# Kernel tuning notes

Hardware: AMD Instinct MI355X
Metric: run time of the kernel (lower is better)

## Reference

```python
import jax, jax.numpy as jnp
import numpy as np

B = 16        # molecules per batch (equal-size segments)
N = 2048      # atoms per molecule
EPS = 1e-09   # module epsilon added to distances
TINY = 1e-16  # jitter inside sqrt to keep grads finite on the masked diagonal


def setup_inputs() -> dict:
    key = jax.random.key(0)
    k1, k2 = jax.random.split(key)
    positions = jax.random.normal(k1, (B * N, 3), dtype=jnp.float32) * 5.0  # [BN,3]
    q = jax.random.normal(k2, (B * N, 1), dtype=jnp.float32)                # [BN,1]
    batch = jnp.repeat(jnp.arange(B, dtype=jnp.int32), N)                   # [BN], sorted equal segments
    return {"positions": positions, "q": q, "batch": batch}


def reference(positions, q, batch):
    # Equal-size segments: the per-molecule python loop in the torch module
    # becomes a batched [B,N,...] computation (batch ids are sorted, N per mol).
    r = positions.reshape(B, N, 3)
    qb = q.reshape(B, N, 1)

    diff = r[:, :, None, :] - r[:, None, :, :]                    # [B,N,N,3]
    dist = jnp.sqrt(jnp.sum(diff * diff, axis=-1) + TINY) + EPS   # [B,N,N]
    dist = dist[..., None]                                        # [B,N,N,1]

    mask = (1.0 - jnp.eye(N, dtype=positions.dtype))[..., None]   # [N,N,1] zero diagonal

    # q_i * q_j / |r_i - r_j|, self-interaction masked, double-count halved
    pot = mask * (qb[:, :, None, :] * qb[:, None, :, :] / dist)   # [B,N,N,1]
    pot_per_mol = pot.sum(axis=(1, 2)) * 0.5                      # [B, n_q=1]
    coulomb_potential = pot_per_mol.sum(axis=1)                   # [B] (aggregation 'sum')

    # field_j = sum_i q_i / |r_i - r_j|  (norm_factor = 1.0)
    field = (qb[:, :, None, :] / dist * mask).sum(axis=1)         # [B,N,1]
    q_field = field.reshape(B * N, 1)                             # [BN,1]

    return coulomb_potential, q_field
```

## Files before the change

### kernel.cpp

```cpp
#include <hip/hip_runtime.h>

#define NB 16
#define NA 2048
#define BLOCK 256
#define JL 8
#define JT 4
#define JB (JL*JT)
#define SPLIT 32
#define RSTRIDE 33

__global__ void zero_pot_kernel(float* out) {
    if (threadIdx.x < NB) out[threadIdx.x] = 0.0f;
}

__global__ __launch_bounds__(BLOCK) void coulomb_kernel(
    const float* __restrict__ pos,
    const float* __restrict__ q,
    float* __restrict__ out)
{
    __shared__ float4 sp4[NA];
    __shared__ float red[SPLIT * RSTRIDE];

    const int t = threadIdx.x;
    const int blocksPerMol = NA / JB;
    const int mol   = blockIdx.x / blocksPerMol;
    const int jBase = (blockIdx.x % blocksPerMol) * JB;
    const long molAtom = (long)mol * NA;

    for (int k = t; k < NA; k += BLOCK) {
        const long a = molAtom + k;
        sp4[k] = make_float4(pos[a*3+0], pos[a*3+1], pos[a*3+2], q[a]);
    }
    __syncthreads();

    const int jl  = t & (JL - 1);
    const int sid = t >> 3;
    const int j0  = jBase + jl;

    float4 jp[JT];
    int    jidx[JT];
    #pragma unroll
    for (int m = 0; m < JT; ++m) {
        jidx[m] = j0 + m * JL;
        jp[m]   = sp4[jidx[m]];
    }

    float acc[JT] = {0.0f, 0.0f, 0.0f, 0.0f};

    #pragma unroll 4
    for (int k = 0; k < NA / SPLIT; ++k) {
        const int i = k * SPLIT + sid;
        const float4 p = sp4[i];
        #pragma unroll
        for (int m = 0; m < JT; ++m) {
            float dx = p.x - jp[m].x;
            float dy = p.y - jp[m].y;
            float dz = p.z - jp[m].z;
            float d2 = fmaf(dx, dx, fmaf(dy, dy, fmaf(dz, dz, 1e-16f)));
            float inv = __builtin_amdgcn_rsqf(d2);
            float qs  = (i == jidx[m]) ? 0.0f : p.w;
            acc[m] = fmaf(qs, inv, acc[m]);
        }
    }

    #pragma unroll
    for (int m = 0; m < JT; ++m)
        red[sid * RSTRIDE + jl + m * JL] = acc[m];
    __syncthreads();

    if (t < JB) {
        float field = 0.0f;
        #pragma unroll
        for (int s = 0; s < SPLIT; ++s) field += red[s * RSTRIDE + t];

        out[NB + molAtom + jBase + t] = field;

        float pot = 0.5f * sp4[jBase + t].w * field;
        #pragma unroll
        for (int off = 16; off > 0; off >>= 1)
            pot += __shfl_down(pot, off, 32);
        if (t == 0) atomicAdd(&out[mol], pot);
    }
}

extern "C" void kernel_launch(void* const* d_in, const int* in_sizes, int n_in,
                              void* d_out, int out_size, void* d_ws, size_t ws_size,
                              hipStream_t stream) {
    const float* pos = (const float*)d_in[0];
    const float* q   = (const float*)d_in[1];
    float* out = (float*)d_out;

    zero_pot_kernel<<<1, 64, 0, stream>>>(out);

    const int grid = NB * (NA / JB);
    coulomb_kernel<<<grid, BLOCK, 0, stream>>>(pos, q, out);
}
```

Baseline: 80.05 us.

## Prepack float4 atoms in workspace and read from global instead of LDS staging

```diff
diff --git a/kernel.cpp b/kernel.cpp
--- a/kernel.cpp
+++ b/kernel.cpp
@@ -7,42 +7,39 @@
 #define JT 4
 #define JB (JL*JT)
 #define SPLIT 32
-#define RSTRIDE 33
 
-__global__ void zero_pot_kernel(float* out) {
-    if (threadIdx.x < NB) out[threadIdx.x] = 0.0f;
+__global__ void pack_zero_kernel(const float* __restrict__ pos,
+                                 const float* __restrict__ q,
+                                 float4* __restrict__ pk,
+                                 float* __restrict__ out) {
+    const int a = blockIdx.x * blockDim.x + threadIdx.x;
+    pk[a] = make_float4(pos[a*3+0], pos[a*3+1], pos[a*3+2], q[a]);
+    if (blockIdx.x == 0 && threadIdx.x < NB) out[threadIdx.x] = 0.0f;
 }
 
 __global__ __launch_bounds__(BLOCK) void coulomb_kernel(
-    const float* __restrict__ pos,
-    const float* __restrict__ q,
+    const float4* __restrict__ pk,
     float* __restrict__ out)
 {
-    __shared__ float4 sp4[NA];
-    __shared__ float red[SPLIT * RSTRIDE];
+    __shared__ float red[4 * JB];
 
     const int t = threadIdx.x;
     const int blocksPerMol = NA / JB;
     const int mol   = blockIdx.x / blocksPerMol;
     const int jBase = (blockIdx.x % blocksPerMol) * JB;
     const long molAtom = (long)mol * NA;
+    const float4* mp = pk + molAtom;
 
-    for (int k = t; k < NA; k += BLOCK) {
-        const long a = molAtom + k;
-        sp4[k] = make_float4(pos[a*3+0], pos[a*3+1], pos[a*3+2], q[a]);
-    }
-    __syncthreads();
-
-    const int jl  = t & (JL - 1);
-    const int sid = t >> 3;
-    const int j0  = jBase + jl;
+    const int jl   = t & (JL - 1);
+    const int sid  = t >> 3;
+    const int wave = t >> 6;
 
     float4 jp[JT];
     int    jidx[JT];
     #pragma unroll
     for (int m = 0; m < JT; ++m) {
-        jidx[m] = j0 + m * JL;
-        jp[m]   = sp4[jidx[m]];
+        jidx[m] = jBase + jl + m * JL;
+        jp[m]   = mp[jidx[m]];
     }
 
     float acc[JT] = {0.0f, 0.0f, 0.0f, 0.0f};
@@ -50,7 +47,7 @@
     #pragma unroll 4
     for (int k = 0; k < NA / SPLIT; ++k) {
         const int i = k * SPLIT + sid;
-        const float4 p = sp4[i];
+        const float4 p = mp[i];
         #pragma unroll
         for (int m = 0; m < JT; ++m) {
             float dx = p.x - jp[m].x;
@@ -64,18 +61,24 @@
     }
 
     #pragma unroll
-    for (int m = 0; m < JT; ++m)
-        red[sid * RSTRIDE + jl + m * JL] = acc[m];
+    for (int m = 0; m < JT; ++m) {
+        acc[m] += __shfl_xor(acc[m], 8,  64);
+        acc[m] += __shfl_xor(acc[m], 16, 64);
+        acc[m] += __shfl_xor(acc[m], 32, 64);
+    }
+    if ((t & 63) < JL) {
+        #pragma unroll
+        for (int m = 0; m < JT; ++m)
+            red[wave * JB + jl + m * JL] = acc[m];
+    }
     __syncthreads();
 
     if (t < JB) {
-        float field = 0.0f;
-        #pragma unroll
-        for (int s = 0; s < SPLIT; ++s) field += red[s * RSTRIDE + t];
+        float field = red[t] + red[JB + t] + red[2*JB + t] + red[3*JB + t];
 
         out[NB + molAtom + jBase + t] = field;
 
-        float pot = 0.5f * sp4[jBase + t].w * field;
+        float pot = 0.5f * mp[jBase + t].w * field;
         #pragma unroll
         for (int off = 16; off > 0; off >>= 1)
             pot += __shfl_down(pot, off, 32);
@@ -89,9 +92,10 @@
     const float* pos = (const float*)d_in[0];
     const float* q   = (const float*)d_in[1];
     float* out = (float*)d_out;
+    float4* pk = (float4*)d_ws;
 
-    zero_pot_kernel<<<1, 64, 0, stream>>>(out);
+    pack_zero_kernel<<<(NB * NA) / BLOCK, BLOCK, 0, stream>>>(pos, q, pk, out);
 
     const int grid = NB * (NA / JB);
-    coulomb_kernel<<<grid, BLOCK, 0, stream>>>(pos, q, out);
+    coulomb_kernel<<<grid, BLOCK, 0, stream>>>(pk, out);
 }
```

Result: slower. 81.85 us (+2.3%).
